# Kernel tuning notes

Measured on AMD Instinct MI355X. Metric: run time of the kernel, lower is better.

## Reference

```python
import jax, jax.numpy as jnp
import numpy as np

B, T, I, H, O = 256, 512, 128, 512, 64
ALPHA = 0.2          # cfg.leak
BETA = 8.0           # cfg.softplus_beta
THRESH = 20.0        # cfg.softplus_threshold


def _phi(x):
    # F.softplus(x, beta, threshold): linear when beta*x > threshold
    z = BETA * x
    return jnp.where(z > THRESH, x, jax.nn.softplus(jnp.minimum(z, THRESH)) / BETA)


def setup_inputs() -> dict:
    key = jax.random.key(0)
    ks = jax.random.split(key, 6)
    x = jax.random.normal(ks[0], (B, T, I), dtype=jnp.float32)
    W_xh = jax.random.normal(ks[1], (H, I), dtype=jnp.float32) * (1.0 / np.sqrt(I))
    # E/I structure: column-wise sign (abs weights * sign), scaled to modest spectral radius
    sign = np.ones(H, dtype=np.float32)
    perm = np.random.default_rng(0).permutation(H)
    sign[perm[int(round(0.8 * H)):]] = -1.0
    W_hh = jnp.abs(jax.random.normal(ks[2], (H, H), dtype=jnp.float32)) * jnp.asarray(sign)[None, :]
    W_hh = W_hh * (1.2 / (jnp.linalg.norm(W_hh, ord=2) + 1e-6))
    b_h = jnp.zeros((H,), dtype=jnp.float32)
    W_out = jax.random.normal(ks[3], (O, H), dtype=jnp.float32) * (1.0 / np.sqrt(H))
    b_out = jnp.zeros((O,), dtype=jnp.float32)
    return {"x": x, "W_xh": W_xh, "W_hh": W_hh, "b_h": b_h, "W_out": W_out, "b_out": b_out}


def reference(x, W_xh, W_hh, b_h, W_out, b_out):
    # precompute input projection: [B,T,H]
    xw = jnp.einsum('bti,hi->bth', x, W_xh)

    def step(h, xw_t):  # h: [B,H], xw_t: [B,H]
        pre = xw_t + h @ W_hh.T + b_h
        h = (1.0 - ALPHA) * h + ALPHA * _phi(pre)
        y = h @ W_out.T + b_out  # readout='all'
        return h, y

    h0 = jnp.zeros((x.shape[0], W_hh.shape[0]), dtype=x.dtype)
    _, ys = jax.lax.scan(step, h0, jnp.swapaxes(xw, 0, 1))  # ys: [T,B,O]
    return jnp.swapaxes(ys, 0, 1)  # [B,T,O]
```

## Files before the change

### kernel.cpp

```cpp
#include <hip/hip_runtime.h>


#define BB 256
#define TT 512
#define II 128
#define HH 512
#define OO 64
#define RG 16
#define JC 64
#define NG 16
#define NC 8

typedef _Float16 f16;
typedef f16 f16x8 __attribute__((ext_vector_type(8)));
typedef float f32x4 __attribute__((ext_vector_type(4)));

__global__ __launch_bounds__(256, 1)
void eirnn_persist(const float* __restrict__ x,
                   const float* __restrict__ Wxh,
                   const float* __restrict__ Whh,
                   const float* __restrict__ bh,
                   const float* __restrict__ Wout,
                   const float* __restrict__ bout,
                   float* __restrict__ yout,
                   f16* __restrict__ hbuf,
                   unsigned int* __restrict__ flg)
{
    const int tid  = threadIdx.x;
    const int bid  = blockIdx.x;
    const int wave = tid >> 6;
    const int lane = tid & 63;
    const int quad = lane >> 4;
    const int l16  = lane & 15;
    const int r    = bid >> 3;
    const int c    = bid & 7;
    const int rowbase = r * RG;
    const int jbase   = c * JC;
    const int myrow   = wave * 16 + l16;

    __shared__ __align__(16) f16 hg[RG][HH + 8];
    __shared__ __align__(16) f16 xsh[RG][II + 8];

    f16x8 bf[16];
    f16x8 xbf[4];
    f16x8 bfo[2];
    {
        const float* wp = Whh + (size_t)(jbase + myrow) * HH + quad * 8;
        #pragma unroll
        for (int ks = 0; ks < 16; ++ks) {
            float4 u = *(const float4*)(wp + ks * 32);
            float4 v = *(const float4*)(wp + ks * 32 + 4);
            f16x8 tv;
            tv[0]=(f16)u.x; tv[1]=(f16)u.y; tv[2]=(f16)u.z; tv[3]=(f16)u.w;
            tv[4]=(f16)v.x; tv[5]=(f16)v.y; tv[6]=(f16)v.z; tv[7]=(f16)v.w;
            bf[ks] = tv;
        }
        const float* wq = Wxh + (size_t)(jbase + myrow) * II + quad * 8;
        #pragma unroll
        for (int ks = 0; ks < 4; ++ks) {
            float4 u = *(const float4*)(wq + ks * 32);
            float4 v = *(const float4*)(wq + ks * 32 + 4);
            f16x8 tv;
            tv[0]=(f16)u.x; tv[1]=(f16)u.y; tv[2]=(f16)u.z; tv[3]=(f16)u.w;
            tv[4]=(f16)v.x; tv[5]=(f16)v.y; tv[6]=(f16)v.z; tv[7]=(f16)v.w;
            xbf[ks] = tv;
        }
        const float* wo = Wout + (size_t)myrow * HH + c * 64 + quad * 8;
        #pragma unroll
        for (int ks = 0; ks < 2; ++ks) {
            float4 u = *(const float4*)(wo + ks * 32);
            float4 v = *(const float4*)(wo + ks * 32 + 4);
            f16x8 tv;
            tv[0]=(f16)u.x; tv[1]=(f16)u.y; tv[2]=(f16)u.z; tv[3]=(f16)u.w;
            tv[4]=(f16)v.x; tv[5]=(f16)v.y; tv[6]=(f16)v.z; tv[7]=(f16)v.w;
            bfo[ks] = tv;
        }
    }
    const float biash = bh[jbase + myrow];
    const float biaso = (c == 0) ? bout[myrow] : 0.0f;

    for (int p = tid; p < RG * (HH + 8) / 2; p += 256)
        ((unsigned int*)hg)[p] = 0u;

    float hreg[4] = {0.f, 0.f, 0.f, 0.f};

    const int col8  = tid & 127;
    const int shard = col8 >> 4;
    const int pw    = (tid & 15) >> 2;
    const int row0  = tid >> 7;
    const unsigned int* fpoll = flg + ((r * NC + shard) * 4 + pw);
    unsigned int* fmine = flg + ((r * NC + c) * 4 + wave);

    float4 xpf0, xpf1;
    {
        int p0 = tid, p1 = tid + 256;
        xpf0 = ((const float4*)(x + ((size_t)(rowbase + (p0 >> 5)) * TT + 0) * II))[p0 & 31];
        xpf1 = ((const float4*)(x + ((size_t)(rowbase + (p1 >> 5)) * TT + 0) * II))[p1 & 31];
    }

    __syncthreads();

    for (int t = 0; t <= TT; ++t) {
        if (t < TT) {
            int p0 = tid, p1 = tid + 256;
            f16* d0 = &xsh[p0 >> 5][(p0 & 31) * 4];
            d0[0]=(f16)xpf0.x; d0[1]=(f16)xpf0.y; d0[2]=(f16)xpf0.z; d0[3]=(f16)xpf0.w;
            f16* d1 = &xsh[p1 >> 5][(p1 & 31) * 4];
            d1[0]=(f16)xpf1.x; d1[1]=(f16)xpf1.y; d1[2]=(f16)xpf1.z; d1[3]=(f16)xpf1.w;
        }
        if (t + 1 < TT) {
            int p0 = tid, p1 = tid + 256;
            xpf0 = ((const float4*)(x + ((size_t)(rowbase + (p0 >> 5)) * TT + (t + 1)) * II))[p0 & 31];
            xpf1 = ((const float4*)(x + ((size_t)(rowbase + (p1 >> 5)) * TT + (t + 1)) * II))[p1 & 31];
        }
        if (t >= 1) {
            while (__hip_atomic_load(fpoll, __ATOMIC_RELAXED, __HIP_MEMORY_SCOPE_AGENT)
                   < (unsigned)t) {}
            const unsigned long long* src = (const unsigned long long*)hbuf
                + (size_t)(t & 1) * (BB * HH / 4) + (size_t)rowbase * (HH / 4) + col8;
            unsigned long long v[8];
            #pragma unroll
            for (int i = 0; i < 8; ++i)
                v[i] = __hip_atomic_load(src + (size_t)(row0 + 2 * i) * (HH / 4),
                                         __ATOMIC_RELAXED, __HIP_MEMORY_SCOPE_AGENT);
            #pragma unroll
            for (int i = 0; i < 8; ++i)
                *(unsigned long long*)&hg[row0 + 2 * i][col8 * 4] = v[i];
        }
        __syncthreads();

        if (t < TT) {
            f32x4 acc0 = {0.f,0.f,0.f,0.f}, acc1 = {0.f,0.f,0.f,0.f};
            #pragma unroll
            for (int ks = 0; ks < 16; ks += 2) {
                f16x8 a0 = *(const f16x8*)&hg[l16][ks * 32 + quad * 8];
                f16x8 a1 = *(const f16x8*)&hg[l16][(ks + 1) * 32 + quad * 8];
                acc0 = __builtin_amdgcn_mfma_f32_16x16x32_f16(a0, bf[ks], acc0, 0, 0, 0);
                acc1 = __builtin_amdgcn_mfma_f32_16x16x32_f16(a1, bf[ks + 1], acc1, 0, 0, 0);
            }
            #pragma unroll
            for (int ks = 0; ks < 4; ks += 2) {
                f16x8 a0 = *(const f16x8*)&xsh[l16][ks * 32 + quad * 8];
                f16x8 a1 = *(const f16x8*)&xsh[l16][(ks + 1) * 32 + quad * 8];
                acc0 = __builtin_amdgcn_mfma_f32_16x16x32_f16(a0, xbf[ks], acc0, 0, 0, 0);
                acc1 = __builtin_amdgcn_mfma_f32_16x16x32_f16(a1, xbf[ks + 1], acc1, 0, 0, 0);
            }
            unsigned int* dstw = (unsigned int*)hbuf + (size_t)((t + 1) & 1) * (BB * HH / 2);
            unsigned int hb[4];
            #pragma unroll
            for (int reg = 0; reg < 4; ++reg) {
                float pre = acc0[reg] + acc1[reg] + biash;
                float z = 8.f * pre;
                float ph = (z > 20.f) ? pre : (__logf(1.f + __expf(z)) * 0.125f);
                float hn = 0.8f * hreg[reg] + 0.2f * ph;
                hreg[reg] = hn;
                hb[reg] = (unsigned int)__builtin_bit_cast(unsigned short, (f16)hn);
            }
            #pragma unroll
            for (int reg = 0; reg < 4; ++reg) {
                unsigned int ob = (unsigned int)__shfl_xor((int)hb[reg], 1, 64);
                if ((lane & 1) == 0) {
                    size_t eidx = (size_t)(rowbase + quad * 4 + reg) * HH + jbase + myrow;
                    __hip_atomic_store(dstw + (eidx >> 1), hb[reg] | (ob << 16),
                                       __ATOMIC_RELAXED, __HIP_MEMORY_SCOPE_AGENT);
                }
            }
            __builtin_amdgcn_s_waitcnt(0);
            if (lane == 0)
                __hip_atomic_store(fmine, (unsigned)(t + 1),
                                   __ATOMIC_RELAXED, __HIP_MEMORY_SCOPE_AGENT);
        }

        if (t >= 1) {
            f32x4 ya = {0.f,0.f,0.f,0.f};
            f16x8 a0 = *(const f16x8*)&hg[l16][c * 64 + quad * 8];
            f16x8 a1 = *(const f16x8*)&hg[l16][c * 64 + 32 + quad * 8];
            ya = __builtin_amdgcn_mfma_f32_16x16x32_f16(a0, bfo[0], ya, 0, 0, 0);
            ya = __builtin_amdgcn_mfma_f32_16x16x32_f16(a1, bfo[1], ya, 0, 0, 0);
            #pragma unroll
            for (int reg = 0; reg < 4; ++reg)
                atomicAdd(yout + ((size_t)(rowbase + quad * 4 + reg) * TT + (t - 1)) * OO + myrow,
                          ya[reg] + biaso);
        }
        __syncthreads();
    }
}

extern "C" void kernel_launch(void* const* d_in, const int* in_sizes, int n_in,
                              void* d_out, int out_size, void* d_ws, size_t ws_size,
                              hipStream_t stream)
{
    const float* x    = (const float*)d_in[0];
    const float* Wxh  = (const float*)d_in[1];
    const float* Whh  = (const float*)d_in[2];
    const float* bh   = (const float*)d_in[3];
    const float* Wout = (const float*)d_in[4];
    const float* bout = (const float*)d_in[5];
    float* yout = (float*)d_out;

    f16* hbuf = (f16*)d_ws;
    const size_t hbuf_bytes = (size_t)2 * BB * HH * sizeof(f16);
    unsigned int* flg = (unsigned int*)((char*)d_ws + hbuf_bytes);
    const size_t flg_bytes = (size_t)NG * NC * 4 * sizeof(unsigned int);

    if (ws_size < hbuf_bytes + flg_bytes) return;

    hipMemsetAsync(flg, 0, flg_bytes, stream);
    hipMemsetAsync(yout, 0, (size_t)out_size * sizeof(float), stream);

    eirnn_persist<<<dim3(NG * NC), dim3(256), 0, stream>>>(
        x, Wxh, Whh, bh, Wout, bout, yout, hbuf, flg);
}
```

Baseline: 1.496 ms.

## Replace flag polling with timestep-tagged hidden-state words and double-buffered LDS

Each exchanged hidden value is stored as a 32-bit word holding the f16 value plus a 16-bit timestep tag. Consumers poll the data words directly, so the separate per-wave flag store, the waitcnt before it and the flag polling go away. The block's own slice is written straight into a double-buffered LDS tile, and the trailing barrier per step is removed. This cuts synchronisation latency on the critical recurrent path, at the cost of twice the global exchange traffic and a reliance on leftover workspace tags never matching the expected step.

```diff
diff --git a/kernel.cpp b/kernel.cpp
--- a/kernel.cpp
+++ b/kernel.cpp
@@ -10,6 +10,8 @@
 #define JC 64
 #define NG 16
 #define NC 8
+#define HGP (HH + 8)
+#define XP  (II + 8)
 
 typedef _Float16 f16;
 typedef f16 f16x8 __attribute__((ext_vector_type(8)));
@@ -23,8 +25,7 @@
                    const float* __restrict__ Wout,
                    const float* __restrict__ bout,
                    float* __restrict__ yout,
-                   f16* __restrict__ hbuf,
-                   unsigned int* __restrict__ flg)
+                   unsigned int* __restrict__ hbuf)
 {
     const int tid  = threadIdx.x;
     const int bid  = blockIdx.x;
@@ -38,8 +39,8 @@
     const int jbase   = c * JC;
     const int myrow   = wave * 16 + l16;
 
-    __shared__ __align__(16) f16 hg[RG][HH + 8];
-    __shared__ __align__(16) f16 xsh[RG][II + 8];
+    __shared__ __align__(16) f16 hg[2][RG][HGP];
+    __shared__ __align__(16) f16 xsh[2][RG][XP];
 
     f16x8 bf[16];
     f16x8 xbf[4];
@@ -79,17 +80,12 @@
     const float biash = bh[jbase + myrow];
     const float biaso = (c == 0) ? bout[myrow] : 0.0f;
 
-    for (int p = tid; p < RG * (HH + 8) / 2; p += 256)
-        ((unsigned int*)hg)[p] = 0u;
+    for (int p = tid; p < RG * HGP / 2; p += 256)
+        ((unsigned int*)hg[0])[p] = 0u;
 
     float hreg[4] = {0.f, 0.f, 0.f, 0.f};
 
-    const int col8  = tid & 127;
-    const int shard = col8 >> 4;
-    const int pw    = (tid & 15) >> 2;
-    const int row0  = tid >> 7;
-    const unsigned int* fpoll = flg + ((r * NC + shard) * 4 + pw);
-    unsigned int* fmine = flg + ((r * NC + c) * 4 + wave);
+    const bool own = ((tid >> 5) == c);
 
     float4 xpf0, xpf1;
     {
@@ -98,34 +94,54 @@
         xpf1 = ((const float4*)(x + ((size_t)(rowbase + (p1 >> 5)) * TT + 0) * II))[p1 & 31];
     }
 
-    __syncthreads();
-
     for (int t = 0; t <= TT; ++t) {
+        const int p = t & 1;
+
         if (t < TT) {
             int p0 = tid, p1 = tid + 256;
-            f16* d0 = &xsh[p0 >> 5][(p0 & 31) * 4];
+            f16* d0 = &xsh[p][p0 >> 5][(p0 & 31) * 4];
             d0[0]=(f16)xpf0.x; d0[1]=(f16)xpf0.y; d0[2]=(f16)xpf0.z; d0[3]=(f16)xpf0.w;
-            f16* d1 = &xsh[p1 >> 5][(p1 & 31) * 4];
+            f16* d1 = &xsh[p][p1 >> 5][(p1 & 31) * 4];
             d1[0]=(f16)xpf1.x; d1[1]=(f16)xpf1.y; d1[2]=(f16)xpf1.z; d1[3]=(f16)xpf1.w;
-        }
-        if (t + 1 < TT) {
-            int p0 = tid, p1 = tid + 256;
-            xpf0 = ((const float4*)(x + ((size_t)(rowbase + (p0 >> 5)) * TT + (t + 1)) * II))[p0 & 31];
-            xpf1 = ((const float4*)(x + ((size_t)(rowbase + (p1 >> 5)) * TT + (t + 1)) * II))[p1 & 31];
-        }
-        if (t >= 1) {
-            while (__hip_atomic_load(fpoll, __ATOMIC_RELAXED, __HIP_MEMORY_SCOPE_AGENT)
-                   < (unsigned)t) {}
+            if (t + 1 < TT) {
+                xpf0 = ((const float4*)(x + ((size_t)(rowbase + (p0 >> 5)) * TT + (t + 1)) * II))[p0 & 31];
+                xpf1 = ((const float4*)(x + ((size_t)(rowbase + (p1 >> 5)) * TT + (t + 1)) * II))[p1 & 31];
+            }
+        }
+
+        if (t >= 1 && !own) {
+            const unsigned tg = (unsigned)t;
             const unsigned long long* src = (const unsigned long long*)hbuf
-                + (size_t)(t & 1) * (BB * HH / 4) + (size_t)rowbase * (HH / 4) + col8;
-            unsigned long long v[8];
-            #pragma unroll
-            for (int i = 0; i < 8; ++i)
-                v[i] = __hip_atomic_load(src + (size_t)(row0 + 2 * i) * (HH / 4),
+                + (size_t)p * (BB * HH / 2) + (size_t)rowbase * (HH / 2) + tid;
+            unsigned long long v[16];
+            #pragma unroll
+            for (int k = 0; k < 16; ++k)
+                v[k] = __hip_atomic_load(src + (size_t)k * (HH / 2),
                                          __ATOMIC_RELAXED, __HIP_MEMORY_SCOPE_AGENT);
-            #pragma unroll
-            for (int i = 0; i < 8; ++i)
-                *(unsigned long long*)&hg[row0 + 2 * i][col8 * 4] = v[i];
+            unsigned pend = 0xffffu;
+            while (pend) {
+                unsigned np = 0;
+                #pragma unroll
+                for (int k = 0; k < 16; ++k) {
+                    if (pend & (1u << k)) {
+                        unsigned lo = (unsigned)v[k];
+                        unsigned hi = (unsigned)(v[k] >> 32);
+                        if (((lo >> 16) == tg) & ((hi >> 16) == tg)) {
+                            *(unsigned int*)&hg[p][k][2 * tid] = (lo & 0xffffu) | (hi << 16);
+                        } else {
+                            np |= (1u << k);
+                        }
+                    }
+                }
+                pend = np;
+                if (np) {
+                    #pragma unroll
+                    for (int k = 0; k < 16; ++k)
+                        if (np & (1u << k))
+                            v[k] = __hip_atomic_load(src + (size_t)k * (HH / 2),
+                                                     __ATOMIC_RELAXED, __HIP_MEMORY_SCOPE_AGENT);
+                }
+            }
         }
         __syncthreads();
 
@@ -133,20 +149,20 @@
             f32x4 acc0 = {0.f,0.f,0.f,0.f}, acc1 = {0.f,0.f,0.f,0.f};
             #pragma unroll
             for (int ks = 0; ks < 16; ks += 2) {
-                f16x8 a0 = *(const f16x8*)&hg[l16][ks * 32 + quad * 8];
-                f16x8 a1 = *(const f16x8*)&hg[l16][(ks + 1) * 32 + quad * 8];
+                f16x8 a0 = *(const f16x8*)&hg[p][l16][ks * 32 + quad * 8];
+                f16x8 a1 = *(const f16x8*)&hg[p][l16][(ks + 1) * 32 + quad * 8];
                 acc0 = __builtin_amdgcn_mfma_f32_16x16x32_f16(a0, bf[ks], acc0, 0, 0, 0);
                 acc1 = __builtin_amdgcn_mfma_f32_16x16x32_f16(a1, bf[ks + 1], acc1, 0, 0, 0);
             }
             #pragma unroll
             for (int ks = 0; ks < 4; ks += 2) {
-                f16x8 a0 = *(const f16x8*)&xsh[l16][ks * 32 + quad * 8];
-                f16x8 a1 = *(const f16x8*)&xsh[l16][(ks + 1) * 32 + quad * 8];
+                f16x8 a0 = *(const f16x8*)&xsh[p][l16][ks * 32 + quad * 8];
+                f16x8 a1 = *(const f16x8*)&xsh[p][l16][(ks + 1) * 32 + quad * 8];
                 acc0 = __builtin_amdgcn_mfma_f32_16x16x32_f16(a0, xbf[ks], acc0, 0, 0, 0);
                 acc1 = __builtin_amdgcn_mfma_f32_16x16x32_f16(a1, xbf[ks + 1], acc1, 0, 0, 0);
             }
-            unsigned int* dstw = (unsigned int*)hbuf + (size_t)((t + 1) & 1) * (BB * HH / 2);
-            unsigned int hb[4];
+            unsigned int* dst = hbuf + (size_t)((t + 1) & 1) * (BB * HH);
+            const unsigned tg1 = (unsigned)(t + 1) << 16;
             #pragma unroll
             for (int reg = 0; reg < 4; ++reg) {
                 float pre = acc0[reg] + acc1[reg] + biash;
@@ -154,27 +170,18 @@
                 float ph = (z > 20.f) ? pre : (__logf(1.f + __expf(z)) * 0.125f);
                 float hn = 0.8f * hreg[reg] + 0.2f * ph;
                 hreg[reg] = hn;
-                hb[reg] = (unsigned int)__builtin_bit_cast(unsigned short, (f16)hn);
-            }
-            #pragma unroll
-            for (int reg = 0; reg < 4; ++reg) {
-                unsigned int ob = (unsigned int)__shfl_xor((int)hb[reg], 1, 64);
-                if ((lane & 1) == 0) {
-                    size_t eidx = (size_t)(rowbase + quad * 4 + reg) * HH + jbase + myrow;
-                    __hip_atomic_store(dstw + (eidx >> 1), hb[reg] | (ob << 16),
-                                       __ATOMIC_RELAXED, __HIP_MEMORY_SCOPE_AGENT);
-                }
-            }
-            __builtin_amdgcn_s_waitcnt(0);
-            if (lane == 0)
-                __hip_atomic_store(fmine, (unsigned)(t + 1),
-                                   __ATOMIC_RELAXED, __HIP_MEMORY_SCOPE_AGENT);
+                f16 h16 = (f16)hn;
+                hg[1 - p][quad * 4 + reg][jbase + myrow] = h16;
+                unsigned hb = (unsigned)__builtin_bit_cast(unsigned short, h16);
+                __hip_atomic_store(dst + (size_t)(rowbase + quad * 4 + reg) * HH + jbase + myrow,
+                                   tg1 | hb, __ATOMIC_RELAXED, __HIP_MEMORY_SCOPE_AGENT);
+            }
         }
 
         if (t >= 1) {
             f32x4 ya = {0.f,0.f,0.f,0.f};
-            f16x8 a0 = *(const f16x8*)&hg[l16][c * 64 + quad * 8];
-            f16x8 a1 = *(const f16x8*)&hg[l16][c * 64 + 32 + quad * 8];
+            f16x8 a0 = *(const f16x8*)&hg[p][l16][c * 64 + quad * 8];
+            f16x8 a1 = *(const f16x8*)&hg[p][l16][c * 64 + 32 + quad * 8];
             ya = __builtin_amdgcn_mfma_f32_16x16x32_f16(a0, bfo[0], ya, 0, 0, 0);
             ya = __builtin_amdgcn_mfma_f32_16x16x32_f16(a1, bfo[1], ya, 0, 0, 0);
             #pragma unroll
@@ -182,7 +189,6 @@
                 atomicAdd(yout + ((size_t)(rowbase + quad * 4 + reg) * TT + (t - 1)) * OO + myrow,
                           ya[reg] + biaso);
         }
-        __syncthreads();
     }
 }
 
@@ -198,16 +204,12 @@
     const float* bout = (const float*)d_in[5];
     float* yout = (float*)d_out;
 
-    f16* hbuf = (f16*)d_ws;
-    const size_t hbuf_bytes = (size_t)2 * BB * HH * sizeof(f16);
-    unsigned int* flg = (unsigned int*)((char*)d_ws + hbuf_bytes);
-    const size_t flg_bytes = (size_t)NG * NC * 4 * sizeof(unsigned int);
-
-    if (ws_size < hbuf_bytes + flg_bytes) return;
-
-    hipMemsetAsync(flg, 0, flg_bytes, stream);
+    unsigned int* hbuf = (unsigned int*)d_ws;
+    const size_t hbuf_bytes = (size_t)2 * BB * HH * sizeof(unsigned int);
+    if (ws_size < hbuf_bytes) return;
+
     hipMemsetAsync(yout, 0, (size_t)out_size * sizeof(float), stream);
 
     eirnn_persist<<<dim3(NG * NC), dim3(256), 0, stream>>>(
-        x, Wxh, Whh, bh, Wout, bout, yout, hbuf, flg);
+        x, Wxh, Whh, bh, Wout, bout, yout, hbuf);
 }
```

After: 1.882 ms. 1.26x slower.
